# Performance work log

Hardware: AMD Instinct MI355X
Metric: run time of the kernel (lower is better)

## Reference

```python
import jax, jax.numpy as jnp
import numpy as np
import math

EMBED_DIM = 2048
NUM_HEADS = 16
D_K = 128
BSZ = 2
SEQ = 2048


def make_freq_pos_enc(dim, max_seq_len):
    # inv_freq over dim/2 freqs, then interleave-repeat each freq twice: (f r), r=2
    inv_freq = 1.0 / (10000.0 ** (jnp.arange(0, dim, 2, dtype=jnp.float32) / dim))
    pos = jnp.arange(max_seq_len, dtype=jnp.float32)
    pe = jnp.einsum('p,f->pf', pos, inv_freq)                 # [S, dim/2]
    return jnp.repeat(pe, 2, axis=-1)                          # [S, dim], pattern (f r)


def rotate_half(u):
    # pairs are interleaved: (..., d r) with r=2
    u = u.reshape(*u.shape[:-1], -1, 2)
    u1, u2 = u[..., 0], u[..., 1]
    return jnp.stack((-u2, u1), axis=-1).reshape(*u.shape[:-2], -1)


def rotate(u, pos_enc):
    pe = pos_enc[: u.shape[-2]]                                # [S, d_k]
    return u * jnp.cos(pe) + rotate_half(u) * jnp.sin(pe)


def setup_inputs() -> dict:
    key = jax.random.key(0)
    ks = jax.random.split(key, 5)
    scale = 1.0 / math.sqrt(EMBED_DIM)
    return {
        'x': jax.random.normal(ks[0], (BSZ, SEQ, EMBED_DIM), dtype=jnp.float32),
        'wq': jax.random.normal(ks[1], (NUM_HEADS * D_K, EMBED_DIM), dtype=jnp.float32) * scale,
        'wk': jax.random.normal(ks[2], (NUM_HEADS * D_K, EMBED_DIM), dtype=jnp.float32) * scale,
        'wv': jax.random.normal(ks[3], (NUM_HEADS * D_K, EMBED_DIM), dtype=jnp.float32) * scale,
        'wo': jax.random.normal(ks[4], (EMBED_DIM, NUM_HEADS * D_K), dtype=jnp.float32) * scale,
        'freq_pos_enc': make_freq_pos_enc(D_K, SEQ),
        'mask': jnp.zeros((SEQ, SEQ), dtype=jnp.float32),  # dead arg in original forward
        'num_heads': NUM_HEADS,
        'd_k': D_K,
    }


def reference(x, wq, wk, wv, wo, freq_pos_enc, mask, num_heads, d_k):
    bsz, seq_len, _ = x.shape
    # projections (nn.Linear, no bias): x @ W^T
    def proj(w):
        p = jnp.einsum('bse,de->bsd', x, w)
        return p.reshape(bsz, seq_len, num_heads, d_k).transpose(0, 2, 1, 3)  # [B,H,S,d]
    q, k, v = proj(wq), proj(wk), proj(wv)
    q, k = rotate(q, freq_pos_enc), rotate(k, freq_pos_enc)
    # regenerated causal mask (0 on/below diagonal, -inf above)
    causal = jnp.where(
        jnp.arange(seq_len)[:, None] >= jnp.arange(seq_len)[None, :],
        0.0, -jnp.inf).astype(x.dtype)
    scores = jnp.einsum('bhsd,bhtd->bhst', q, k) / math.sqrt(d_k) + causal
    weights = jax.nn.softmax(scores, axis=-1)
    attn = jnp.einsum('bhst,bhtd->bhsd', weights, v)           # [B,H,S,d]
    attn = attn.transpose(0, 2, 1, 3).reshape(bsz, seq_len, -1)
    return jnp.einsum('bsd,ed->bse', attn, wo)


if __name__ == '__main__':
    out = reference(**setup_inputs())
    print(out.shape, out.dtype)
```

## Files before the change

### kernel.cpp

```cpp
#include <hip/hip_runtime.h>


typedef unsigned short u16;
typedef unsigned int   u32;
typedef __attribute__((ext_vector_type(4)))  float f32x4;
typedef __attribute__((ext_vector_type(16))) float f32x16;
typedef __attribute__((ext_vector_type(8)))  short short8;
typedef __attribute__((ext_vector_type(4)))  u16   u16x4;
typedef __attribute__((ext_vector_type(2)))  u16   u16x2;

#define NB   2
#define NH   16
#define SEQ  2048
#define DK   128
#define EMB  2048

__device__ __forceinline__ u16 f2bf(float f) {
    union { float f; unsigned int u; } v; v.f = f;
    unsigned int r = v.u + 0x7FFFu + ((v.u >> 16) & 1u);
    return (u16)(r >> 16);
}
__device__ __forceinline__ float bf2f(u16 h) {
    union { unsigned int u; float f; } v; v.u = ((unsigned int)h) << 16;
    return v.f;
}
__device__ __forceinline__ f32x4 mfma16(short8 a, short8 b, f32x4 c) {
    return __builtin_amdgcn_mfma_f32_16x16x32_bf16(a, b, c, 0, 0, 0);
}
__device__ __forceinline__ f32x16 mfma32(short8 a, short8 b, f32x16 c) {
    return __builtin_amdgcn_mfma_f32_32x32x16_bf16(a, b, c, 0, 0, 0);
}

#define GLDS(gsrc, ldst) __builtin_amdgcn_global_load_lds( \
    (const __attribute__((address_space(1))) void*)(gsrc), \
    (__attribute__((address_space(3))) void*)(ldst), 16, 0, 0)

__global__ __launch_bounds__(256) void cast_f32_bf16(const float* __restrict__ in,
                                                     u16* __restrict__ out, int n4) {
    int i = blockIdx.x * 256 + threadIdx.x;
    if (i >= n4) return;
    f32x4 v = ((const f32x4*)in)[i];
    u16x4 o;
    o[0] = f2bf(v[0]); o[1] = f2bf(v[1]); o[2] = f2bf(v[2]); o[3] = f2bf(v[3]);
    ((u16x4*)out)[i] = o;
}

__global__ __launch_bounds__(256) void cast_weights(const float* __restrict__ wq,
                                                    const float* __restrict__ wk,
                                                    const float* __restrict__ wv,
                                                    const float* __restrict__ wo,
                                                    u16* __restrict__ oq, u16* __restrict__ ok,
                                                    u16* __restrict__ ov, u16* __restrict__ oo) {
    int i   = blockIdx.x * 256 + threadIdx.x;
    int sel = i >> 20;
    int idx = i & 1048575;
    const float* src = (sel == 0) ? wq : (sel == 1) ? wk : (sel == 2) ? wv : wo;
    u16*         dst = (sel == 0) ? oq : (sel == 1) ? ok : (sel == 2) ? ov : oo;
    f32x4 v = ((const f32x4*)src)[idx];
    u16x4 o;
    o[0] = f2bf(v[0]); o[1] = f2bf(v[1]); o[2] = f2bf(v[2]); o[3] = f2bf(v[3]);
    ((u16x4*)dst)[idx] = o;
}

__global__ __launch_bounds__(256) void rope_table(const float* __restrict__ freq,
                                                  float* __restrict__ ct,
                                                  float* __restrict__ st) {
    int i = blockIdx.x * 256 + threadIdx.x;
    int s = i >> 6, d2 = i & 63;
    float pe = freq[s * DK + d2 * 2];
    ct[i] = cosf(pe);
    st[i] = sinf(pe);
}

template <int MODE>
__global__ __launch_bounds__(256) void gemm_ring(const u16* __restrict__ A,
                                                 const u16* __restrict__ B,
                                                 void* __restrict__ Cout,
                                                 int M, int N, int K,
                                                 const float* __restrict__ ct,
                                                 const float* __restrict__ st) {
    __shared__ __align__(16) u16 As[3 * 4096];
    __shared__ __align__(16) u16 Bs[3 * 4096];
    const int tid  = threadIdx.x;
    const int lane = tid & 63;
    const int wid  = tid >> 6;
    const int wm   = wid >> 1, wn = wid & 1;
    const int nwgx = (int)gridDim.x;
    const int wgid = (int)blockIdx.y * nwgx + (int)blockIdx.x;
    const int cpx  = (nwgx * (int)gridDim.y) >> 3;
    const int swz  = (wgid & 7) * cpx + (wgid >> 3);
    const int m0   = (swz % nwgx) * 128, n0 = (swz / nwgx) * 128;
    const int lr   = lane & 15, lk = lane >> 4;

    const u16* Asrc = A + (size_t)(m0 + (tid >> 2)) * K + (tid & 3) * 8;
    const u16* Bsrc = B + (size_t)(n0 + (tid >> 2)) * K + (tid & 3) * 8;
    const int  dst0 = wid * 512;

    f32x4 acc[4][4] = {};
    const int NT = K >> 5;

#pragma unroll
    for (int i = 0; i < 2; ++i) {
        GLDS(Asrc + (size_t)i * 64 * K,      &As[i * 2048 + dst0]);
        GLDS(Bsrc + (size_t)i * 64 * K,      &Bs[i * 2048 + dst0]);
    }
#pragma unroll
    for (int i = 0; i < 2; ++i) {
        GLDS(Asrc + (size_t)i * 64 * K + 32, &As[4096 + i * 2048 + dst0]);
        GLDS(Bsrc + (size_t)i * 64 * K + 32, &Bs[4096 + i * 2048 + dst0]);
    }

    int buf = 0;
    for (int t = 0; t < NT; ++t) {
        if (t < NT - 1) asm volatile("s_waitcnt vmcnt(4)" ::: "memory");
        else            asm volatile("s_waitcnt vmcnt(0)" ::: "memory");
        __builtin_amdgcn_s_barrier();

        short8 af[4], bf[4];
#pragma unroll
        for (int i = 0; i < 4; ++i)
            af[i] = *(const short8*)&As[buf * 4096 + (wm * 64 + i * 16 + lr) * 32 + lk * 8];
#pragma unroll
        for (int j = 0; j < 4; ++j)
            bf[j] = *(const short8*)&Bs[buf * 4096 + (wn * 64 + j * 16 + lr) * 32 + lk * 8];

        if (t + 2 < NT) {
            int b2 = buf + 2; if (b2 >= 3) b2 -= 3;
            const u16* a2  = Asrc + (size_t)(t + 2) * 32;
            const u16* b2p = Bsrc + (size_t)(t + 2) * 32;
#pragma unroll
            for (int i = 0; i < 2; ++i) {
                GLDS(a2  + (size_t)i * 64 * K, &As[b2 * 4096 + i * 2048 + dst0]);
                GLDS(b2p + (size_t)i * 64 * K, &Bs[b2 * 4096 + i * 2048 + dst0]);
            }
        }

        __builtin_amdgcn_s_setprio(1);
#pragma unroll
        for (int i = 0; i < 4; ++i)
#pragma unroll
            for (int j = 0; j < 4; ++j)
                acc[i][j] = mfma16(af[i], bf[j], acc[i][j]);
        __builtin_amdgcn_s_setprio(0);

        buf = (buf == 2) ? 0 : buf + 1;
    }

#pragma unroll
    for (int i = 0; i < 4; ++i) {
#pragma unroll
        for (int j = 0; j < 4; ++j) {
#pragma unroll
            for (int r = 0; r < 4; ++r) {
                int m = m0 + wm * 64 + i * 16 + lk * 4 + r;
                int n = n0 + wn * 64 + j * 16 + lr;
                float v = acc[i][j][r];
                if (MODE == 0) {
                    int b = m >> 11, s = m & (SEQ - 1), h = n >> 7, d = n & (DK - 1);
                    ((u16*)Cout)[(((size_t)(b * NH + h) * SEQ + s) * DK) + d] = f2bf(v);
                } else if (MODE == 1) {
                    int h = m >> 7, d = m & (DK - 1), b = n >> 11, s = n & (SEQ - 1);
                    ((u16*)Cout)[(((size_t)(b * NH + h) * DK + d) * SEQ) + s] = f2bf(v);
                } else if (MODE == 6) {
                    int b = m >> 11, s = m & (SEQ - 1), h = n >> 7, d = n & (DK - 1);
                    float part = __shfl_xor(v, 1);
                    int ti = (s << 6) + (d >> 1);
                    float c = ct[ti], sn = st[ti];
                    float vr = (lr & 1) ? (v * c + part * sn) : (v * c - part * sn);
                    ((u16*)Cout)[(((size_t)(b * NH + h) * SEQ + s) * DK) + d] = f2bf(vr);
                } else {
                    ((float*)Cout)[(size_t)m * N + n] = v;
                }
            }
        }
    }
}

__global__ __launch_bounds__(128, 2) void attn_lds2(const u16* __restrict__ Q,
                                                    const u16* __restrict__ K,
                                                    const u16* __restrict__ VT,
                                                    u16* __restrict__ O) {
    const int gid  = blockIdx.x;
    const int bh   = (gid & 7) * 4 + ((gid >> 3) & 3);
    const int p    = 31 - (gid >> 5);
    const int tid  = threadIdx.x;
    const int w    = tid >> 6;
    const int l    = tid & 63;
    const int q32  = l & 31;
    const int half = l >> 5;
    const int qc   = 2 * p + w;
    const int nt   = 2 * p + 2;
    const int q0   = qc * 32;

    __shared__ __align__(16) u16 Ksh[2][4096];
    __shared__ __align__(16) u16 Vsh[2][4096];

    const u16* Kg  = K  + (size_t)bh * SEQ * DK;
    const u16* VTg = VT + (size_t)bh * DK * SEQ;
    const int b = bh >> 4, h = bh & 15;

    auto stage = [&](int t, int bufn) {
#pragma unroll
        for (int i = 0; i < 4; ++i) {
            int cid = i * 128 + w * 64 + l;
            int kr = cid >> 4, kc = cid & 15;
            GLDS(Kg + (size_t)(t * 32 + kr) * DK + ((kc ^ (kr & 7)) * 8),
                 &Ksh[bufn][(i * 128 + w * 64) * 8]);
            int vr = cid >> 2, vc = cid & 3;
            GLDS(VTg + (size_t)vr * SEQ + t * 32 + ((vc ^ ((vr >> 1) & 3)) * 8),
                 &Vsh[bufn][(i * 128 + w * 64) * 8]);
        }
    };

    short8 qf[8];
    {
        const u16* Qg = Q + ((size_t)bh * SEQ + q0) * DK;
#pragma unroll
        for (int kq = 0; kq < 8; ++kq)
            qf[kq] = *(const short8*)(Qg + q32 * DK + kq * 16 + half * 8);
    }

    f32x16 oacc[4] = {};
    float m = -INFINITY, lsum = 0.f;

    stage(0, 0);
    stage(1, 1);
    for (int t = 0; t < nt; ++t) {
        const int buf = t & 1;
        if (t + 1 < nt) asm volatile("s_waitcnt vmcnt(8)" ::: "memory");
        else            asm volatile("s_waitcnt vmcnt(0)" ::: "memory");
        __builtin_amdgcn_s_barrier();
        __builtin_amdgcn_sched_barrier(0);

        if (t <= qc) {
            const float rs = 0.08838834764831845f;
            short8 kf[8], vf[8];
#pragma unroll
            for (int kq = 0; kq < 8; ++kq) {
                int c = (kq * 2 + half) ^ (q32 & 7);
                kf[kq] = *(const short8*)&Ksh[buf][q32 * 128 + c * 8];
            }
#pragma unroll
            for (int i = 0; i < 8; ++i) {
                int dblk = i >> 1, ch = i & 1;
                int vrow = dblk * 32 + q32;
                int c = (ch * 2 + half) ^ ((q32 >> 1) & 3);
                vf[i] = *(const short8*)&Vsh[buf][vrow * 32 + c * 8];
            }
            const bool diag = (t == qc);

            f32x16 sacc = {};
            __builtin_amdgcn_s_setprio(1);
#pragma unroll
            for (int kq = 0; kq < 8; ++kq) sacc = mfma32(kf[kq], qf[kq], sacc);
            __builtin_amdgcn_s_setprio(0);
#pragma unroll
            for (int r = 0; r < 16; ++r) {
                int kk = (r & 3) + 8 * (r >> 2) + 4 * half;
                float s = sacc[r] * rs;
                if (diag && kk > q32) s = -INFINITY;
                sacc[r] = s;
            }
            float mx[8];
#pragma unroll
            for (int r = 0; r < 8; ++r) mx[r] = fmaxf(sacc[r], sacc[r + 8]);
#pragma unroll
            for (int r = 0; r < 4; ++r) mx[r] = fmaxf(mx[r], mx[r + 4]);
            float tmax = fmaxf(fmaxf(mx[0], mx[1]), fmaxf(mx[2], mx[3]));
            tmax = fmaxf(tmax, __shfl_xor(tmax, 32));
            if (__any(tmax - m > 8.0f)) {
                float mn = fmaxf(m, tmax);
                float sc = __expf(m - mn);
                m = mn; lsum *= sc;
#pragma unroll
                for (int d = 0; d < 4; ++d)
#pragma unroll
                    for (int r = 0; r < 16; ++r) oacc[d][r] *= sc;
            }
#pragma unroll
            for (int r = 0; r < 16; ++r) sacc[r] = __expf(sacc[r] - m);
            float sm[8];
#pragma unroll
            for (int r = 0; r < 8; ++r) sm[r] = sacc[r] + sacc[r + 8];
#pragma unroll
            for (int r = 0; r < 4; ++r) sm[r] = sm[r] + sm[r + 4];
            float tsum = (sm[0] + sm[1]) + (sm[2] + sm[3]);
            tsum += __shfl_xor(tsum, 32);
            lsum += tsum;
            u32 pk[8];
#pragma unroll
            for (int i = 0; i < 8; ++i)
                pk[i] = ((u32)f2bf(sacc[2 * i + 1]) << 16) | (u32)f2bf(sacc[2 * i]);
            u32 s0 = __shfl_xor((int)pk[0], 32), s1 = __shfl_xor((int)pk[1], 32);
            u32 s2 = __shfl_xor((int)pk[2], 32), s3 = __shfl_xor((int)pk[3], 32);
            u32 s4 = __shfl_xor((int)pk[4], 32), s5 = __shfl_xor((int)pk[5], 32);
            u32 s6 = __shfl_xor((int)pk[6], 32), s7 = __shfl_xor((int)pk[7], 32);
            union { u32 wd[4]; short8 s8; } P0, P1;
            P0.wd[0] = half ? s2    : pk[0];  P0.wd[1] = half ? s3    : pk[1];
            P0.wd[2] = half ? pk[2] : s0;     P0.wd[3] = half ? pk[3] : s1;
            P1.wd[0] = half ? s6    : pk[4];  P1.wd[1] = half ? s7    : pk[5];
            P1.wd[2] = half ? pk[6] : s4;     P1.wd[3] = half ? pk[7] : s5;
            __builtin_amdgcn_s_setprio(1);
#pragma unroll
            for (int d = 0; d < 4; ++d) {
                oacc[d] = mfma32(vf[2 * d],     P0.s8, oacc[d]);
                oacc[d] = mfma32(vf[2 * d + 1], P1.s8, oacc[d]);
            }
            __builtin_amdgcn_s_setprio(0);
        }

        __builtin_amdgcn_s_barrier();
        if (t + 2 < nt) stage(t + 2, buf);
    }

    float inv = 1.0f / lsum;
    u16* Og = O + ((size_t)b * SEQ + q0 + q32) * EMB + h * DK;
#pragma unroll
    for (int d = 0; d < 4; ++d)
#pragma unroll
        for (int rq = 0; rq < 4; ++rq) {
            u16x4 o4;
#pragma unroll
            for (int j = 0; j < 4; ++j) o4[j] = f2bf(oacc[d][rq * 4 + j] * inv);
            *(u16x4*)(Og + d * 32 + rq * 8 + half * 4) = o4;
        }
}

extern "C" void kernel_launch(void* const* d_in, const int* in_sizes, int n_in,
                              void* d_out, int out_size, void* d_ws, size_t ws_size,
                              hipStream_t stream) {
    const float* x    = (const float*)d_in[0];
    const float* wq   = (const float*)d_in[1];
    const float* wk   = (const float*)d_in[2];
    const float* wv   = (const float*)d_in[3];
    const float* wo   = (const float*)d_in[4];
    const float* freq = (const float*)d_in[5];

    char* ws = (char*)d_ws;
    u16*  xb  = (u16*)(ws);
    u16*  wqb = (u16*)(ws + 16777216);
    u16*  wkb = (u16*)(ws + 25165824);
    u16*  wvb = (u16*)(ws + 33554432);
    u16*  wob = (u16*)(ws + 41943040);
    u16*  Qb  = (u16*)(ws + 50331648);
    u16*  Kb  = (u16*)(ws + 67108864);
    u16*  VTb = (u16*)(ws + 83886080);
    float* ct = (float*)(ws + 100663296);
    float* st = (float*)(ws + 101187584);
    u16*  attn = xb;

    cast_f32_bf16<<<8192, 256, 0, stream>>>(x, xb, 2097152);
    cast_weights<<<16384, 256, 0, stream>>>(wq, wk, wv, wo, wqb, wkb, wvb, wob);
    rope_table<<<512, 256, 0, stream>>>(freq, ct, st);

    gemm_ring<6><<<dim3(32, 16), 256, 0, stream>>>(xb,  wqb, Qb,  4096, 2048, 2048, ct, st);
    gemm_ring<6><<<dim3(32, 16), 256, 0, stream>>>(xb,  wkb, Kb,  4096, 2048, 2048, ct, st);
    gemm_ring<1><<<dim3(16, 32), 256, 0, stream>>>(wvb, xb,  VTb, 2048, 4096, 2048, nullptr, nullptr);

    attn_lds2<<<1024, 128, 0, stream>>>(Qb, Kb, VTb, attn);

    gemm_ring<3><<<dim3(32, 16), 256, 0, stream>>>(attn, wob, d_out, 4096, 2048, 2048, nullptr, nullptr);
}
```

Measured before the change: 285.4 us.

## Fuse Q/K/V projection GEMMs into one launch and defer softmax row-sum shuffle

Merges the three separate projection GEMM launches (Q and K with fused RoPE, V transposed) into a single 1536-workgroup kernel that picks its operands and epilogue from the block index. This removes launch gaps and the tail underutilization of three 512-block grids, letting the projections overlap on the GPU. Separately, the attention kernel now accumulates per-half partial row sums and does the cross-half shuffle once at the end instead of every tile. The specialized output GEMM is split out with a plain fp32 epilogue.

```diff
diff --git a/kernel.cpp b/kernel.cpp
--- a/kernel.cpp
+++ b/kernel.cpp
@@ -72,13 +72,119 @@
     st[i] = sinf(pe);
 }
 
-template <int MODE>
-__global__ __launch_bounds__(256) void gemm_ring(const u16* __restrict__ A,
-                                                 const u16* __restrict__ B,
-                                                 void* __restrict__ Cout,
-                                                 int M, int N, int K,
+__global__ __launch_bounds__(256) void gemm_proj(const u16* __restrict__ xb,
+                                                 const u16* __restrict__ wqb,
+                                                 const u16* __restrict__ wkb,
+                                                 const u16* __restrict__ wvb,
+                                                 u16* __restrict__ Qb,
+                                                 u16* __restrict__ Kb,
+                                                 u16* __restrict__ VTb,
                                                  const float* __restrict__ ct,
                                                  const float* __restrict__ st) {
+    __shared__ __align__(16) u16 As[3 * 4096];
+    __shared__ __align__(16) u16 Bs[3 * 4096];
+    const int gid  = blockIdx.x;
+    const int grp  = gid >> 9;
+    const int lg   = gid & 511;
+    const int tid  = threadIdx.x;
+    const int lane = tid & 63;
+    const int wid  = tid >> 6;
+    const int wm   = wid >> 1, wn = wid & 1;
+    const int swz  = (lg & 7) * 64 + (lg >> 3);
+    const int K    = 2048;
+
+    int m0, n0;
+    const u16 *A, *B;
+    if (grp < 2) { m0 = (swz & 31) * 128;  n0 = (swz >> 5) * 128;
+                   A = xb;  B = grp ? wkb : wqb; }
+    else         { m0 = (swz & 15) * 128;  n0 = (swz >> 4) * 128;
+                   A = wvb; B = xb; }
+    const int lr   = lane & 15, lk = lane >> 4;
+
+    const u16* Asrc = A + (size_t)(m0 + (tid >> 2)) * K + (tid & 3) * 8;
+    const u16* Bsrc = B + (size_t)(n0 + (tid >> 2)) * K + (tid & 3) * 8;
+    const int  dst0 = wid * 512;
+
+    f32x4 acc[4][4] = {};
+    const int NT = K >> 5;
+
+#pragma unroll
+    for (int i = 0; i < 2; ++i) {
+        GLDS(Asrc + (size_t)i * 64 * K,      &As[i * 2048 + dst0]);
+        GLDS(Bsrc + (size_t)i * 64 * K,      &Bs[i * 2048 + dst0]);
+    }
+#pragma unroll
+    for (int i = 0; i < 2; ++i) {
+        GLDS(Asrc + (size_t)i * 64 * K + 32, &As[4096 + i * 2048 + dst0]);
+        GLDS(Bsrc + (size_t)i * 64 * K + 32, &Bs[4096 + i * 2048 + dst0]);
+    }
+
+    int buf = 0;
+    for (int t = 0; t < NT; ++t) {
+        if (t < NT - 1) asm volatile("s_waitcnt vmcnt(4)" ::: "memory");
+        else            asm volatile("s_waitcnt vmcnt(0)" ::: "memory");
+        __builtin_amdgcn_s_barrier();
+
+        short8 af[4], bf[4];
+#pragma unroll
+        for (int i = 0; i < 4; ++i)
+            af[i] = *(const short8*)&As[buf * 4096 + (wm * 64 + i * 16 + lr) * 32 + lk * 8];
+#pragma unroll
+        for (int j = 0; j < 4; ++j)
+            bf[j] = *(const short8*)&Bs[buf * 4096 + (wn * 64 + j * 16 + lr) * 32 + lk * 8];
+
+        if (t + 2 < NT) {
+            int b2 = buf + 2; if (b2 >= 3) b2 -= 3;
+            const u16* a2  = Asrc + (size_t)(t + 2) * 32;
+            const u16* b2p = Bsrc + (size_t)(t + 2) * 32;
+#pragma unroll
+            for (int i = 0; i < 2; ++i) {
+                GLDS(a2  + (size_t)i * 64 * K, &As[b2 * 4096 + i * 2048 + dst0]);
+                GLDS(b2p + (size_t)i * 64 * K, &Bs[b2 * 4096 + i * 2048 + dst0]);
+            }
+        }
+
+        __builtin_amdgcn_s_setprio(1);
+#pragma unroll
+        for (int i = 0; i < 4; ++i)
+#pragma unroll
+            for (int j = 0; j < 4; ++j)
+                acc[i][j] = mfma16(af[i], bf[j], acc[i][j]);
+        __builtin_amdgcn_s_setprio(0);
+
+        buf = (buf == 2) ? 0 : buf + 1;
+    }
+
+#pragma unroll
+    for (int i = 0; i < 4; ++i) {
+#pragma unroll
+        for (int j = 0; j < 4; ++j) {
+#pragma unroll
+            for (int r = 0; r < 4; ++r) {
+                int m = m0 + wm * 64 + i * 16 + lk * 4 + r;
+                int n = n0 + wn * 64 + j * 16 + lr;
+                float v = acc[i][j][r];
+                if (grp < 2) {
+                    int b = m >> 11, s = m & (SEQ - 1), h = n >> 7, d = n & (DK - 1);
+                    float part = __shfl_xor(v, 1);
+                    int ti = (s << 6) + (d >> 1);
+                    float c = ct[ti], sn = st[ti];
+                    float vr = (lr & 1) ? (v * c + part * sn) : (v * c - part * sn);
+                    u16* Cb = grp ? Kb : Qb;
+                    Cb[(((size_t)(b * NH + h) * SEQ + s) * DK) + d] = f2bf(vr);
+                } else {
+                    int h = m >> 7, d = m & (DK - 1), b = n >> 11, s = n & (SEQ - 1);
+                    VTb[(((size_t)(b * NH + h) * DK + d) * SEQ) + s] = f2bf(v);
+                }
+            }
+        }
+    }
+}
+
+__global__ __launch_bounds__(256) void gemm_out(const u16* __restrict__ A,
+                                                const u16* __restrict__ B,
+                                                float* __restrict__ Cout,
+                                                int M, int N, int K) {
     __shared__ __align__(16) u16 As[3 * 4096];
     __shared__ __align__(16) u16 Bs[3 * 4096];
     const int tid  = threadIdx.x;
@@ -147,33 +253,15 @@
     }
 
 #pragma unroll
-    for (int i = 0; i < 4; ++i) {
-#pragma unroll
-        for (int j = 0; j < 4; ++j) {
+    for (int i = 0; i < 4; ++i)
+#pragma unroll
+        for (int j = 0; j < 4; ++j)
 #pragma unroll
             for (int r = 0; r < 4; ++r) {
                 int m = m0 + wm * 64 + i * 16 + lk * 4 + r;
                 int n = n0 + wn * 64 + j * 16 + lr;
-                float v = acc[i][j][r];
-                if (MODE == 0) {
-                    int b = m >> 11, s = m & (SEQ - 1), h = n >> 7, d = n & (DK - 1);
-                    ((u16*)Cout)[(((size_t)(b * NH + h) * SEQ + s) * DK) + d] = f2bf(v);
-                } else if (MODE == 1) {
-                    int h = m >> 7, d = m & (DK - 1), b = n >> 11, s = n & (SEQ - 1);
-                    ((u16*)Cout)[(((size_t)(b * NH + h) * DK + d) * SEQ) + s] = f2bf(v);
-                } else if (MODE == 6) {
-                    int b = m >> 11, s = m & (SEQ - 1), h = n >> 7, d = n & (DK - 1);
-                    float part = __shfl_xor(v, 1);
-                    int ti = (s << 6) + (d >> 1);
-                    float c = ct[ti], sn = st[ti];
-                    float vr = (lr & 1) ? (v * c + part * sn) : (v * c - part * sn);
-                    ((u16*)Cout)[(((size_t)(b * NH + h) * SEQ + s) * DK) + d] = f2bf(vr);
-                } else {
-                    ((float*)Cout)[(size_t)m * N + n] = v;
-                }
-            }
-        }
-    }
+                Cout[(size_t)m * N + n] = acc[i][j][r];
+            }
 }
 
 __global__ __launch_bounds__(128, 2) void attn_lds2(const u16* __restrict__ Q,
@@ -284,9 +372,7 @@
             for (int r = 0; r < 8; ++r) sm[r] = sacc[r] + sacc[r + 8];
 #pragma unroll
             for (int r = 0; r < 4; ++r) sm[r] = sm[r] + sm[r + 4];
-            float tsum = (sm[0] + sm[1]) + (sm[2] + sm[3]);
-            tsum += __shfl_xor(tsum, 32);
-            lsum += tsum;
+            lsum += (sm[0] + sm[1]) + (sm[2] + sm[3]);
             u32 pk[8];
 #pragma unroll
             for (int i = 0; i < 8; ++i)
@@ -313,6 +399,7 @@
         if (t + 2 < nt) stage(t + 2, buf);
     }
 
+    lsum += __shfl_xor(lsum, 32);
     float inv = 1.0f / lsum;
     u16* Og = O + ((size_t)b * SEQ + q0 + q32) * EMB + h * DK;
 #pragma unroll
@@ -353,11 +440,9 @@
     cast_weights<<<16384, 256, 0, stream>>>(wq, wk, wv, wo, wqb, wkb, wvb, wob);
     rope_table<<<512, 256, 0, stream>>>(freq, ct, st);
 
-    gemm_ring<6><<<dim3(32, 16), 256, 0, stream>>>(xb,  wqb, Qb,  4096, 2048, 2048, ct, st);
-    gemm_ring<6><<<dim3(32, 16), 256, 0, stream>>>(xb,  wkb, Kb,  4096, 2048, 2048, ct, st);
-    gemm_ring<1><<<dim3(16, 32), 256, 0, stream>>>(wvb, xb,  VTb, 2048, 4096, 2048, nullptr, nullptr);
+    gemm_proj<<<1536, 256, 0, stream>>>(xb, wqb, wkb, wvb, Qb, Kb, VTb, ct, st);
 
     attn_lds2<<<1024, 128, 0, stream>>>(Qb, Kb, VTb, attn);
 
-    gemm_ring<3><<<dim3(32, 16), 256, 0, stream>>>(attn, wob, d_out, 4096, 2048, 2048, nullptr, nullptr);
-}
+    gemm_out<<<dim3(32, 16), 256, 0, stream>>>(attn, wob, (float*)d_out, 4096, 2048, 2048);
+}
```

New measurement: 294.7 us. 3.3% more time.
